# Optimization experiments

Measured on AMD Instinct MI355X. Metric: run time of the kernel, lower is better.

The kernel has to match this reference:

```python
import jax, jax.numpy as jnp
import numpy as np

N = 100000
E = 1600000
IN_C = 128
HID = 256
K_EIG = 64
OUT_C = 16


def setup_inputs() -> dict:
    key = jax.random.key(0)
    ks = jax.random.split(key, 8)
    x = jax.random.normal(ks[0], (N, IN_C), dtype=jnp.float32)
    edge_index = jax.random.randint(ks[1], (2, E), 0, N)
    MLP_W = jax.random.normal(ks[2], (K_EIG, N), dtype=jnp.float32) * 0.02
    MLP_b = jax.random.normal(ks[3], (K_EIG,), dtype=jnp.float32) * 0.02
    mlpx_W = jax.random.normal(ks[4], (HID, IN_C), dtype=jnp.float32) * 0.05
    mlpx_b = jax.random.normal(ks[5], (HID,), dtype=jnp.float32) * 0.02
    fin_W = jax.random.normal(ks[6], (OUT_C, HID + K_EIG), dtype=jnp.float32) * 0.05
    fin_b = jax.random.normal(ks[7], (OUT_C,), dtype=jnp.float32) * 0.02
    return {"x": x, "edge_index": edge_index, "MLP_W": MLP_W, "MLP_b": MLP_b,
            "mlpx_W": mlpx_W, "mlpx_b": mlpx_b, "fin_W": fin_W, "fin_b": fin_b}


def _spmm(row, col, feats, n):
    # adj is COO with coords (col[e], row[e]) and value 1 -> out[col] += feats[row]
    return jax.ops.segment_sum(feats[row], col, num_segments=n)


def _pump(xA, row, col, n):
    # MinCut-style pump: soft assignment, normalized-cut loss + orthogonality loss
    S = jax.nn.softmax(xA, axis=-1)                      # [N, K]
    AS = _spmm(row, col, S, n)                            # A @ S, [N, K]
    cut = jnp.sum(S * AS)                                 # tr(S^T A S)
    deg = jax.ops.segment_sum(jnp.ones(col.shape, S.dtype), col, num_segments=n)
    deg_term = jnp.sum(deg[:, None] * S * S)              # tr(S^T D S)
    pump_loss = -(cut / deg_term)
    SS = S.T @ S                                          # [K, K]
    k = S.shape[1]
    ortho_loss = jnp.linalg.norm(SS / jnp.linalg.norm(SS)
                                 - jnp.eye(k, dtype=S.dtype) / jnp.sqrt(jnp.asarray(k, S.dtype)))
    return S, pump_loss, ortho_loss


def reference(x, edge_index, MLP_W, MLP_b, mlpx_W, mlpx_b, fin_W, fin_b):
    row, col = edge_index[0], edge_index[1]
    n = x.shape[0]
    # xA = adj @ MLP.weight.T + bias   (irregular gather/scatter over edges)
    xA = _spmm(row, col, MLP_W.T, n) + MLP_b              # [N, K]
    xX = x @ mlpx_W.T + mlpx_b                            # [N, HID]
    xA, pump_loss, ortho_loss = _pump(xA, row, col, n)
    z = jnp.concatenate([xX, xA], axis=1)                 # [N, HID+K]
    # dropout omitted (eval mode)
    z = jax.nn.log_softmax(z @ fin_W.T + fin_b, axis=-1)  # [N, OUT]
    return (z, pump_loss + ortho_loss)
```

## Files before the change

### kernel.cpp

```cpp
#include <hip/hip_runtime.h>
#include <math.h>

#define N_NODES 100000
#define N_EDGES 1600000
#define IN_C    128
#define HID     256
#define KEIG    64
#define OUT_C   16

#define NPB      256
#define NBUCKET  ((N_NODES + NPB - 1) / NPB)
#define EDGE_TILE 4096
#define NTILE    ((N_EDGES + EDGE_TILE - 1) / EDGE_TILE)
#define CAP      8960

#define TRANS_BLOCKS   ((N_NODES + 63) / 64)
#define GATHER_BLOCKS  2048
#define CUT_BLOCKS     2048
#define SSP_BLOCKS     512
#define OUTG_BLOCKS    384
#define TAIL_BLOCKS    (128 * 23)

typedef __attribute__((ext_vector_type(8))) short short8;
typedef __attribute__((ext_vector_type(4))) float f32x4;
typedef __attribute__((ext_vector_type(2))) float f32x2;

__device__ __forceinline__ float wave_sum(float v) {
#pragma unroll
    for (int m = 32; m; m >>= 1) v += __shfl_xor(v, m, 64);
    return v;
}
__device__ __forceinline__ float bf2f(unsigned int u) {
    return __uint_as_float((u & 0xffffu) << 16);
}
__device__ __forceinline__ unsigned short f2bf(float f) {
    unsigned int u = __float_as_uint(f);
    u += 0x7fff + ((u >> 16) & 1);
    return (unsigned short)(u >> 16);
}
__device__ __forceinline__ unsigned char f2fp8(float f) {
    int p = __builtin_amdgcn_cvt_pk_fp8_f32(f, f, 0, false);
    return (unsigned char)(p & 0xff);
}

#define FMA4(P, s, W) \
    P.x = fmaf(s, W.x, P.x); P.y = fmaf(s, W.y, P.y); \
    P.z = fmaf(s, W.z, P.z); P.w = fmaf(s, W.w, P.w);

#define GSEL(RR) (q == 0 ? RR.x : q == 1 ? RR.y : q == 2 ? RR.z : RR.w)

#define GATHER4V(TBL, DST) do {                                                  \
    int4 ra_ = *(const int4*)(csr_row + ps + j);                                 \
    int r0_ = GSEL(ra_);                                                         \
    unsigned u0_ = *(const unsigned*)(TBL + (unsigned)r0_ * 64u + cb);           \
    f32x2 p_;                                                                    \
    p_ = __builtin_amdgcn_cvt_pk_f32_fp8(u0_, false); DST.x += p_.x; DST.y += p_.y; \
    p_ = __builtin_amdgcn_cvt_pk_f32_fp8(u0_, true);  DST.z += p_.x; DST.w += p_.y; \
} while (0)

#define GATHER16V(TBL, DST) do {                                                 \
    int4 ra_ = *(const int4*)(csr_row + ps + j);                                 \
    int4 rb_ = *(const int4*)(csr_row + ps + j + 4);                             \
    int4 rc_ = *(const int4*)(csr_row + ps + j + 8);                             \
    int4 rd_ = *(const int4*)(csr_row + ps + j + 12);                            \
    int r0_ = GSEL(ra_), r1_ = GSEL(rb_), r2_ = GSEL(rc_), r3_ = GSEL(rd_);      \
    unsigned u0_ = *(const unsigned*)(TBL + (unsigned)r0_ * 64u + cb);           \
    unsigned u1_ = *(const unsigned*)(TBL + (unsigned)r1_ * 64u + cb);           \
    unsigned u2_ = *(const unsigned*)(TBL + (unsigned)r2_ * 64u + cb);           \
    unsigned u3_ = *(const unsigned*)(TBL + (unsigned)r3_ * 64u + cb);           \
    f32x2 p_;                                                                    \
    p_ = __builtin_amdgcn_cvt_pk_f32_fp8(u0_, false); DST.x += p_.x; DST.y += p_.y; \
    p_ = __builtin_amdgcn_cvt_pk_f32_fp8(u0_, true);  DST.z += p_.x; DST.w += p_.y; \
    p_ = __builtin_amdgcn_cvt_pk_f32_fp8(u1_, false); DST.x += p_.x; DST.y += p_.y; \
    p_ = __builtin_amdgcn_cvt_pk_f32_fp8(u1_, true);  DST.z += p_.x; DST.w += p_.y; \
    p_ = __builtin_amdgcn_cvt_pk_f32_fp8(u2_, false); DST.x += p_.x; DST.y += p_.y; \
    p_ = __builtin_amdgcn_cvt_pk_f32_fp8(u2_, true);  DST.z += p_.x; DST.w += p_.y; \
    p_ = __builtin_amdgcn_cvt_pk_f32_fp8(u3_, false); DST.x += p_.x; DST.y += p_.y; \
    p_ = __builtin_amdgcn_cvt_pk_f32_fp8(u3_, true);  DST.z += p_.x; DST.w += p_.y; \
} while (0)

__global__ void prep_weff(const float* __restrict__ mlpxW, const float* __restrict__ mlpxb,
                          const float* __restrict__ finW, const float* __restrict__ finb,
                          float* __restrict__ Weff, float* __restrict__ beff,
                          int* __restrict__ bcnt, unsigned char* __restrict__ WT8,
                          unsigned char* __restrict__ S8, int* __restrict__ gpad) {
    int t = blockIdx.x * blockDim.x + threadIdx.x;
    const int NW = (IN_C + KEIG) * OUT_C;
    if (t < NW) {
        int k = t >> 4, o = t & 15;
        float acc;
        if (k < IN_C) {
            acc = 0.f;
            for (int c = 0; c < HID; ++c)
                acc += mlpxW[c * IN_C + k] * finW[o * (HID + KEIG) + c];
        } else {
            acc = finW[o * (HID + KEIG) + HID + (k - IN_C)];
        }
        Weff[k * OUT_C + o] = acc;
    }
    int tb = t - NW;
    if (tb >= 0 && tb < OUT_C) {
        float acc = finb[tb];
        for (int c = 0; c < HID; ++c) acc += mlpxb[c] * finW[tb * (HID + KEIG) + c];
        beff[tb] = acc;
    }
    int tz = t - (NW + OUT_C);
    if (tz >= 0 && tz <= NBUCKET) bcnt[tz] = 0;
    int tp = t - (NW + OUT_C + NBUCKET + 1);
    if (tp >= 0 && tp < 16) {
        ((int*)(WT8 + (size_t)N_NODES * 64))[tp] = 0;
        ((int*)(S8 + (size_t)N_NODES * 64))[tp] = 0;
        if (tp == 0) *gpad = 0;
    }
}

__global__ __launch_bounds__(256) void fused_prep(const float* __restrict__ W,
                                                  unsigned char* __restrict__ WT8,
                                                  const int* __restrict__ ei,
                                                  int* __restrict__ bcnt) {
    __shared__ __align__(16) char sm[64 * 65 * 4];
    int t = threadIdx.x;
    if (blockIdx.x < TRANS_BLOCKS) {
        float (*tile)[65] = (float (*)[65])sm;
        int n0 = blockIdx.x * 64;
        int tn = t & 63, tq = t >> 6;
#pragma unroll
        for (int kk = 0; kk < 16; ++kk) {
            int k = tq * 16 + kk;
            int n = n0 + tn;
            tile[k][tn] = (n < N_NODES) ? W[(long long)k * N_NODES + n] : 0.f;
        }
        __syncthreads();
        int tk = t & 63;
#pragma unroll
        for (int ii = 0; ii < 16; ++ii) {
            int n = n0 + tq * 16 + ii;
            if (n < N_NODES) WT8[(unsigned)n * 64u + tk] = f2fp8(tile[tk][tq * 16 + ii] * 32.f);
        }
    } else {
        int* h = (int*)sm;
        for (int i = t; i < NBUCKET; i += 256) h[i] = 0;
        __syncthreads();
        int tile_i = blockIdx.x - TRANS_BLOCKS;
        int e0 = tile_i * EDGE_TILE;
        int e1 = min(e0 + EDGE_TILE, N_EDGES);
        for (int e = e0 + t; e < e1; e += 256)
            atomicAdd(&h[ei[N_EDGES + e] >> 8], 1);
        __syncthreads();
        for (int i = t; i < NBUCKET; i += 256)
            if (h[i]) atomicAdd(&bcnt[i], h[i]);
    }
}

__global__ void bucket_scan(const int* __restrict__ bcnt, int* __restrict__ bbase,
                            int* __restrict__ bcur) {
    __shared__ int sh[512];
    int t = threadIdx.x;
    int v = (t < NBUCKET) ? bcnt[t] : 0;
    sh[t] = v;
    __syncthreads();
    for (int d = 1; d < 512; d <<= 1) {
        int u = (t >= d) ? sh[t - d] : 0;
        __syncthreads();
        sh[t] += u;
        __syncthreads();
    }
    if (t < NBUCKET) { bbase[t] = sh[t] - v; bcur[t] = sh[t] - v; }
    if (t == 0) bbase[NBUCKET] = N_EDGES;
}

__global__ void bucket_scatter(const int* __restrict__ ei, int* __restrict__ bcur,
                               int* __restrict__ ebuf) {
    __shared__ int h[NBUCKET];
    __shared__ int gb[NBUCKET];
    __shared__ int lpre[NBUCKET];
    __shared__ int psum[256];
    __shared__ int stage[EDGE_TILE];
    __shared__ short bkt[EDGE_TILE];
    int t = threadIdx.x;
    for (int i = t; i < NBUCKET; i += 256) h[i] = 0;
    __syncthreads();
    int e0 = blockIdx.x * EDGE_TILE;
    int e1 = min(e0 + EDGE_TILE, N_EDGES);
    int nt = e1 - e0;
    for (int e = e0 + t; e < e1; e += 256)
        atomicAdd(&h[ei[N_EDGES + e] >> 8], 1);
    __syncthreads();
    int a0 = (2 * t < NBUCKET) ? h[2 * t] : 0;
    int a1 = (2 * t + 1 < NBUCKET) ? h[2 * t + 1] : 0;
    psum[t] = a0 + a1;
    __syncthreads();
    for (int d = 1; d < 256; d <<= 1) {
        int u = (t >= d) ? psum[t - d] : 0;
        __syncthreads();
        psum[t] += u;
        __syncthreads();
    }
    int base = (t == 0) ? 0 : psum[t - 1];
    if (2 * t < NBUCKET) lpre[2 * t] = base;
    if (2 * t + 1 < NBUCKET) lpre[2 * t + 1] = base + a0;
    __syncthreads();
    for (int i = t; i < NBUCKET; i += 256) {
        int c = h[i];
        gb[i] = c ? atomicAdd(&bcur[i], c) : 0;
        h[i] = lpre[i];
    }
    __syncthreads();
    for (int e = e0 + t; e < e1; e += 256) {
        int r = ei[e];
        int c = ei[N_EDGES + e];
        int b = c >> 8;
        int slot = atomicAdd(&h[b], 1);
        stage[slot] = r | ((c & 255) << 17);
        bkt[slot] = (short)b;
    }
    __syncthreads();
    for (int s = t; s < nt; s += 256) {
        int b = bkt[s];
        ebuf[gb[b] + s - lpre[b]] = stage[s];
    }
}

__global__ void csr_build(const int* __restrict__ ebuf, const int* __restrict__ bbase,
                          int2* __restrict__ nodei,
                          int* __restrict__ csr_row, int* __restrict__ gpad) {
    __shared__ int hist[NPB];
    __shared__ int sh[NPB];
    __shared__ int curs[NPB];
    __shared__ int staged[CAP];
    __shared__ int pbase_sh;
    int b = blockIdx.x;
    int t = threadIdx.x;
    int s0 = bbase[b], s1 = bbase[b + 1];
    hist[t] = 0;
    __syncthreads();
    for (int i = s0 + t; i < s1; i += 256)
        atomicAdd(&hist[ebuf[i] >> 17], 1);
    __syncthreads();
    int v = hist[t];
    int pv = (v + 3) & ~3;
    sh[t] = pv;
    __syncthreads();
    for (int d = 1; d < 256; d <<= 1) {
        int u = (t >= d) ? sh[t - d] : 0;
        __syncthreads();
        sh[t] += u;
        __syncthreads();
    }
    int pexcl = sh[t] - pv;
    int pt = sh[255];
    if (t == 0) pbase_sh = atomicAdd(gpad, pt);
    __syncthreads();
    int pbase = pbase_sh;
    int node = b * NPB + t;
    if (node < N_NODES) nodei[node] = make_int2(v, pbase + pexcl);
    curs[t] = pexcl;
    __syncthreads();
    if (pt <= CAP) {
        for (int i = t; i < pt; i += 256) staged[i] = N_NODES;
        __syncthreads();
        for (int i = s0 + t; i < s1; i += 256) {
            int pk = ebuf[i];
            int pos = atomicAdd(&curs[pk >> 17], 1);
            staged[pos] = pk & 0x1FFFF;
        }
        __syncthreads();
        for (int i = t; i < pt; i += 256) csr_row[pbase + i] = staged[i];
    } else {
        for (int i = t; i < pt; i += 256) csr_row[pbase + i] = N_NODES;
        __syncthreads();
        for (int i = s0 + t; i < s1; i += 256) {
            int pk = ebuf[i];
            int pos = atomicAdd(&curs[pk >> 17], 1);
            csr_row[pbase + pos] = pk & 0x1FFFF;
        }
    }
}

__global__ void gather_softmax(const int2* __restrict__ nodei,
                               const int* __restrict__ csr_row,
                               const unsigned char* __restrict__ WT8,
                               const float* __restrict__ MLPb,
                               unsigned short* __restrict__ Sb,
                               unsigned char* __restrict__ S8,
                               float* __restrict__ dtp) {
    int lane = threadIdx.x & 63;
    int q = lane >> 4;
    unsigned cb = (unsigned)(lane & 15) * 4u;
    int wib = __builtin_amdgcn_readfirstlane(threadIdx.x >> 6);
    int gw = blockIdx.x * 4 + wib;
    int nw = gridDim.x * 4;
    f32x4 bias = *(const f32x4*)(MLPb + (lane & 15) * 4);
    float dacc = 0.f;
    for (int n = gw; n < N_NODES; n += nw) {
        int2 di = nodei[n];
        int deg = __builtin_amdgcn_readfirstlane(di.x);
        int ps  = __builtin_amdgcn_readfirstlane(di.y);
        int plen = (deg + 3) & ~3;
        f32x4 acc = {0.f, 0.f, 0.f, 0.f};
        int j = 0;
        for (; j + 16 <= plen; j += 16) { GATHER16V(WT8, acc); }
        for (; j < plen; j += 4) { GATHER4V(WT8, acc); }
#pragma unroll
        for (int mm = 16; mm < 64; mm <<= 1) {
            acc.x += __shfl_xor(acc.x, mm, 64);
            acc.y += __shfl_xor(acc.y, mm, 64);
            acc.z += __shfl_xor(acc.z, mm, 64);
            acc.w += __shfl_xor(acc.w, mm, 64);
        }
        float ax = bias.x + acc.x * 0.03125f;
        float ay = bias.y + acc.y * 0.03125f;
        float az = bias.z + acc.z * 0.03125f;
        float aw = bias.w + acc.w * 0.03125f;
        float m4 = fmaxf(fmaxf(ax, ay), fmaxf(az, aw));
#pragma unroll
        for (int mm = 1; mm < 16; mm <<= 1) m4 = fmaxf(m4, __shfl_xor(m4, mm, 64));
        float ex = __expf(ax - m4), ey = __expf(ay - m4);
        float ez = __expf(az - m4), ew = __expf(aw - m4);
        float s4 = (ex + ey) + (ez + ew);
#pragma unroll
        for (int mm = 1; mm < 16; mm <<= 1) s4 += __shfl_xor(s4, mm, 64);
        float inv = 1.f / s4;
        float sx = ex * inv, sy = ey * inv, sz = ez * inv, sw = ew * inv;
        if (q == 0) {
            unsigned lo = (unsigned)f2bf(sx) | ((unsigned)f2bf(sy) << 16);
            unsigned hi = (unsigned)f2bf(sz) | ((unsigned)f2bf(sw) << 16);
            *(uint2*)(Sb + (unsigned)n * 64u + cb) = make_uint2(lo, hi);
            int p8 = __builtin_amdgcn_cvt_pk_fp8_f32(sx * 64.f, sy * 64.f, 0, false);
            p8 = __builtin_amdgcn_cvt_pk_fp8_f32(sz * 64.f, sw * 64.f, p8, true);
            *(unsigned*)(S8 + (unsigned)n * 64u + cb) = (unsigned)p8;
        }
        dacc += (float)deg * ((sx * sx + sy * sy) + (sz * sz + sw * sw));
    }
    dacc = wave_sum(dacc);
    __shared__ float red[4];
    if (lane == 0) red[wib] = dacc * 0.25f;
    __syncthreads();
    if (threadIdx.x == 0) dtp[blockIdx.x] = red[0] + red[1] + red[2] + red[3];
}

__global__ __launch_bounds__(256) void fused_tail(
        const int2* __restrict__ nodei,
        const int* __restrict__ csr_row,
        const unsigned short* __restrict__ Sb, const unsigned char* __restrict__ S8,
        float* __restrict__ cutp, float* __restrict__ ssp,
        const float* __restrict__ x, const float* __restrict__ Weff,
        const float* __restrict__ beff, float* __restrict__ out) {
    __shared__ __align__(16) char sm[768 * 16 + 64];
    int t = threadIdx.x;
    int grp = blockIdx.x / 23;
    int r23 = blockIdx.x % 23;

    if (r23 < 16) {
        int bid = grp * 16 + r23;
        int lane = t & 63;
        int q = lane >> 4;
        unsigned cb = (unsigned)(lane & 15) * 4u;
        int wib = __builtin_amdgcn_readfirstlane(t >> 6);
        int gw = bid * 4 + wib;
        int nw = CUT_BLOCKS * 4;
        float acc = 0.f;
        for (int n = gw; n < N_NODES; n += nw) {
            int2 di = nodei[n];
            int deg = __builtin_amdgcn_readfirstlane(di.x);
            int ps  = __builtin_amdgcn_readfirstlane(di.y);
            uint2 su = *(const uint2*)(Sb + (unsigned)n * 64u + cb);
            int plen = (deg + 3) & ~3;
            f32x4 g = {0.f, 0.f, 0.f, 0.f};
            int j = 0;
            for (; j + 16 <= plen; j += 16) { GATHER16V(S8, g); }
            for (; j < plen; j += 4) { GATHER4V(S8, g); }
            acc += bf2f(su.x) * g.x + bf2f(su.x >> 16) * g.y
                 + bf2f(su.y) * g.z + bf2f(su.y >> 16) * g.w;
        }
        acc = wave_sum(acc);
        float* red = (float*)sm;
        if (lane == 0) red[wib] = acc * 0.015625f;
        __syncthreads();
        if (t == 0) cutp[bid] = red[0] + red[1] + red[2] + red[3];
    } else if (r23 < 20) {
        int bid2 = grp * 4 + (r23 - 16);
        unsigned short (*Sr)[66] = (unsigned short (*)[66])sm;
        int lane = t & 63;
        int w = t >> 6;
        int m = lane & 15;
        int quad = lane >> 4;
        int srow = t >> 3;
        int spart = t & 7;
        f32x4 a0 = {0.f,0.f,0.f,0.f}, a1 = {0.f,0.f,0.f,0.f};
        f32x4 a2 = {0.f,0.f,0.f,0.f}, a3 = {0.f,0.f,0.f,0.f};
        for (int base = bid2 * 32; base < N_NODES; base += SSP_BLOCKS * 32) {
            const uint4* g = (const uint4*)(Sb + (long long)(base + srow) * 64 + spart * 8);
            uint4 d = *g;
            __syncthreads();
            unsigned int* rowp = (unsigned int*)&Sr[srow][0];
            rowp[spart * 4 + 0] = d.x;
            rowp[spart * 4 + 1] = d.y;
            rowp[spart * 4 + 2] = d.z;
            rowp[spart * 4 + 3] = d.w;
            __syncthreads();
            short8 f0, f1, f2, f3;
#pragma unroll
            for (int j = 0; j < 8; ++j) {
                int k = quad * 8 + j;
                f0[j] = (short)Sr[k][m];
                f1[j] = (short)Sr[k][16 + m];
                f2[j] = (short)Sr[k][32 + m];
                f3[j] = (short)Sr[k][48 + m];
            }
            short8 fa = (w == 0) ? f0 : (w == 1) ? f1 : (w == 2) ? f2 : f3;
            a0 = __builtin_amdgcn_mfma_f32_16x16x32_bf16(fa, f0, a0, 0, 0, 0);
            a1 = __builtin_amdgcn_mfma_f32_16x16x32_bf16(fa, f1, a1, 0, 0, 0);
            a2 = __builtin_amdgcn_mfma_f32_16x16x32_bf16(fa, f2, a2, 0, 0, 0);
            a3 = __builtin_amdgcn_mfma_f32_16x16x32_bf16(fa, f3, a3, 0, 0, 0);
        }
        float* dst = ssp + (size_t)bid2 * 4096;
#pragma unroll
        for (int r = 0; r < 4; ++r) {
            int row = w * 16 + quad * 4 + r;
            dst[row * 64 +  0 + m] = a0[r];
            dst[row * 64 + 16 + m] = a1[r];
            dst[row * 64 + 32 + m] = a2[r];
            dst[row * 64 + 48 + m] = a3[r];
        }
    } else {
        int obid = grp * 3 + (r23 - 20);
        float4* Wsh = (float4*)sm;
        float* bsh = (float*)(sm + 768 * 16);
        const float4* W4 = (const float4*)Weff;
        for (int i = t; i < 768; i += 256) Wsh[i] = W4[i];
        if (t < 16) bsh[t] = beff[t];
        __syncthreads();
        for (int r = obid * 256 + t; r < N_NODES; r += OUTG_BLOCKS * 256) {
            float4 p0 = make_float4(bsh[0], bsh[1], bsh[2], bsh[3]);
            float4 p1 = make_float4(bsh[4], bsh[5], bsh[6], bsh[7]);
            float4 p2 = make_float4(bsh[8], bsh[9], bsh[10], bsh[11]);
            float4 p3 = make_float4(bsh[12], bsh[13], bsh[14], bsh[15]);
            const float4* xr = (const float4*)(x + (long long)r * IN_C);
#pragma unroll 8
            for (int j = 0; j < 32; ++j) {
                float4 xv = xr[j];
                int k = j * 4;
                float xs[4] = {xv.x, xv.y, xv.z, xv.w};
#pragma unroll
                for (int c = 0; c < 4; ++c) {
                    float s = xs[c];
                    float4 w0 = Wsh[(k + c) * 4 + 0];
                    float4 w1 = Wsh[(k + c) * 4 + 1];
                    float4 w2 = Wsh[(k + c) * 4 + 2];
                    float4 w3 = Wsh[(k + c) * 4 + 3];
                    FMA4(p0, s, w0); FMA4(p1, s, w1); FMA4(p2, s, w2); FMA4(p3, s, w3);
                }
            }
            const uint2* sr = (const uint2*)(Sb + (long long)r * 64);
#pragma unroll 8
            for (int j = 0; j < 16; ++j) {
                uint2 u = sr[j];
                float xs[4] = {bf2f(u.x), bf2f(u.x >> 16), bf2f(u.y), bf2f(u.y >> 16)};
                int k = IN_C + j * 4;
#pragma unroll
                for (int c = 0; c < 4; ++c) {
                    float s = xs[c];
                    float4 w0 = Wsh[(k + c) * 4 + 0];
                    float4 w1 = Wsh[(k + c) * 4 + 1];
                    float4 w2 = Wsh[(k + c) * 4 + 2];
                    float4 w3 = Wsh[(k + c) * 4 + 3];
                    FMA4(p0, s, w0); FMA4(p1, s, w1); FMA4(p2, s, w2); FMA4(p3, s, w3);
                }
            }
            float m = fmaxf(fmaxf(fmaxf(p0.x, p0.y), fmaxf(p0.z, p0.w)),
                            fmaxf(fmaxf(fmaxf(p1.x, p1.y), fmaxf(p1.z, p1.w)),
                                  fmaxf(fmaxf(fmaxf(p2.x, p2.y), fmaxf(p2.z, p2.w)),
                                        fmaxf(fmaxf(p3.x, p3.y), fmaxf(p3.z, p3.w)))));
            float sum = __expf(p0.x - m) + __expf(p0.y - m) + __expf(p0.z - m) + __expf(p0.w - m)
                      + __expf(p1.x - m) + __expf(p1.y - m) + __expf(p1.z - m) + __expf(p1.w - m)
                      + __expf(p2.x - m) + __expf(p2.y - m) + __expf(p2.z - m) + __expf(p2.w - m)
                      + __expf(p3.x - m) + __expf(p3.y - m) + __expf(p3.z - m) + __expf(p3.w - m);
            float lse = m + logf(sum);
            float4* o4 = (float4*)(out + (long long)r * OUT_C);
            o4[0] = make_float4(p0.x - lse, p0.y - lse, p0.z - lse, p0.w - lse);
            o4[1] = make_float4(p1.x - lse, p1.y - lse, p1.z - lse, p1.w - lse);
            o4[2] = make_float4(p2.x - lse, p2.y - lse, p2.z - lse, p2.w - lse);
            o4[3] = make_float4(p3.x - lse, p3.y - lse, p3.z - lse, p3.w - lse);
        }
    }
}

__global__ void reduce_ss(const float* __restrict__ ssp, float* __restrict__ SS) {
    int e = blockIdx.x * blockDim.x + threadIdx.x;
    float s = 0.f;
    for (int p = 0; p < SSP_BLOCKS; ++p) s += ssp[(size_t)p * 4096 + e];
    SS[e] = s;
}

__global__ void scalars_kernel(const float* __restrict__ cutp, const float* __restrict__ dtp,
                               const float* __restrict__ SS, float* __restrict__ out) {
    __shared__ float red[256];
    int t = threadIdx.x;
    float c = 0.f;
    for (int i = t; i < CUT_BLOCKS; i += 256) c += cutp[i];
    red[t] = c; __syncthreads();
    for (int s = 128; s; s >>= 1) { if (t < s) red[t] += red[t + s]; __syncthreads(); }
    float cut = red[0]; __syncthreads();

    float d = 0.f;
    for (int i = t; i < GATHER_BLOCKS; i += 256) d += dtp[i];
    red[t] = d; __syncthreads();
    for (int s = 128; s; s >>= 1) { if (t < s) red[t] += red[t + s]; __syncthreads(); }
    float dterm = red[0]; __syncthreads();

    float ss[16];
    float sq = 0.f;
#pragma unroll
    for (int j = 0; j < 16; ++j) { ss[j] = SS[t * 16 + j]; sq += ss[j] * ss[j]; }
    red[t] = sq; __syncthreads();
    for (int s = 128; s; s >>= 1) { if (t < s) red[t] += red[t + s]; __syncthreads(); }
    float nrm = sqrtf(red[0]); __syncthreads();

    float osq = 0.f;
#pragma unroll
    for (int j = 0; j < 16; ++j) {
        int idx = t * 16 + j;
        float v = ss[j] / nrm - ((idx % 65 == 0) ? 0.125f : 0.f);
        osq += v * v;
    }
    red[t] = osq; __syncthreads();
    for (int s = 128; s; s >>= 1) { if (t < s) red[t] += red[t + s]; __syncthreads(); }
    if (t == 0) {
        float loss = -(cut / dterm) + sqrtf(red[0]);
        out[(long long)N_NODES * OUT_C] = loss;
    }
}

extern "C" void kernel_launch(void* const* d_in, const int* in_sizes, int n_in,
                              void* d_out, int out_size, void* d_ws, size_t ws_size,
                              hipStream_t stream) {
    const float* x     = (const float*)d_in[0];
    const int*   ei    = (const int*)d_in[1];
    const float* MLPW  = (const float*)d_in[2];
    const float* MLPb  = (const float*)d_in[3];
    const float* mlpxW = (const float*)d_in[4];
    const float* mlpxb = (const float*)d_in[5];
    const float* finW  = (const float*)d_in[6];
    const float* finb  = (const float*)d_in[7];
    float* out = (float*)d_out;
    char* ws = (char*)d_ws;

    unsigned char*  WT8 = (unsigned char*)ws;
    unsigned char*  S8  = (unsigned char*)(ws + (size_t)(N_NODES + 1) * 64);
    unsigned short* Sb  = (unsigned short*)(ws + (size_t)(N_NODES + 1) * 128);
    char* p = ws + (size_t)(N_NODES + 1) * 128 + (size_t)N_NODES * 128;
    float* ssp  = (float*)p;
    float* SS   = ssp + (size_t)SSP_BLOCKS * 4096;
    float* Weff = SS + 4096;
    float* beff = Weff + 192 * 16;
    float* cutp = beff + 16;
    float* dtp  = cutp + CUT_BLOCKS;
    int* ebuf    = (int*)(dtp + GATHER_BLOCKS);
    int* csr_row = ebuf + N_EDGES;
    int2* nodei  = (int2*)(csr_row + N_EDGES + 16 * N_NODES);
    int* bcnt    = (int*)(nodei + N_NODES);
    int* bbase   = bcnt + NBUCKET + 1;
    int* bcur    = bbase + NBUCKET + 1;
    int* gpad    = bcur + NBUCKET;

    hipLaunchKernelGGL(prep_weff, dim3(16), dim3(256), 0, stream,
                       mlpxW, mlpxb, finW, finb, Weff, beff, bcnt, WT8, S8, gpad);
    hipLaunchKernelGGL(fused_prep, dim3(TRANS_BLOCKS + NTILE), dim3(256), 0, stream,
                       MLPW, WT8, ei, bcnt);
    hipLaunchKernelGGL(bucket_scan, dim3(1), dim3(512), 0, stream, bcnt, bbase, bcur);
    hipLaunchKernelGGL(bucket_scatter, dim3(NTILE), dim3(256), 0, stream, ei, bcur, ebuf);
    hipLaunchKernelGGL(csr_build, dim3(NBUCKET), dim3(256), 0, stream,
                       ebuf, bbase, nodei, csr_row, gpad);
    hipLaunchKernelGGL(gather_softmax, dim3(GATHER_BLOCKS), dim3(256), 0, stream,
                       nodei, csr_row, WT8, MLPb, Sb, S8, dtp);
    hipLaunchKernelGGL(fused_tail, dim3(TAIL_BLOCKS), dim3(256), 0, stream,
                       nodei, csr_row, Sb, S8, cutp, ssp, x, Weff, beff, out);
    hipLaunchKernelGGL(reduce_ss, dim3(16), dim3(256), 0, stream, ssp, SS);
    hipLaunchKernelGGL(scalars_kernel, dim3(1), dim3(256), 0, stream, cutp, dtp, SS, out);
}
```

Before: 305.2 us.

## Software-pipeline CSR gathers over contiguous 16-node wave chunks with 16-padded rows

The gather kernels stop striding one node per wave. Each wave now owns a contiguous chunk of 16 nodes whose padded CSR rows form one run, and it walks that run in groups of 16 edges. Index loads are prefetched two groups ahead and table loads one group ahead, which hides the latency of the dependent index-then-row loads. CSR row padding goes from 4 to 16, the grid sizes and tail block split are rebalanced, and launch bounds are added. The larger padding adds wasted sentinel gathers for low-degree nodes, and contiguous chunking can cause load imbalance across waves.

```diff
diff --git a/kernel.cpp b/kernel.cpp
--- a/kernel.cpp
+++ b/kernel.cpp
@@ -15,11 +15,12 @@
 #define CAP      8960
 
 #define TRANS_BLOCKS   ((N_NODES + 63) / 64)
-#define GATHER_BLOCKS  2048
-#define CUT_BLOCKS     2048
-#define SSP_BLOCKS     512
-#define OUTG_BLOCKS    384
-#define TAIL_BLOCKS    (128 * 23)
+#define GATHER_BLOCKS  ((N_NODES + 63) / 64)
+#define CUT_VB         1573
+#define SSP_BLOCKS     484
+#define SSP_ALLOC      512
+#define OUTG_BLOCKS    363
+#define TAIL_BLOCKS    (121 * 20)
 
 typedef __attribute__((ext_vector_type(8))) short short8;
 typedef __attribute__((ext_vector_type(4))) float f32x4;
@@ -47,36 +48,15 @@
     P.x = fmaf(s, W.x, P.x); P.y = fmaf(s, W.y, P.y); \
     P.z = fmaf(s, W.z, P.z); P.w = fmaf(s, W.w, P.w);
 
-#define GSEL(RR) (q == 0 ? RR.x : q == 1 ? RR.y : q == 2 ? RR.z : RR.w)
-
-#define GATHER4V(TBL, DST) do {                                                  \
-    int4 ra_ = *(const int4*)(csr_row + ps + j);                                 \
-    int r0_ = GSEL(ra_);                                                         \
-    unsigned u0_ = *(const unsigned*)(TBL + (unsigned)r0_ * 64u + cb);           \
-    f32x2 p_;                                                                    \
-    p_ = __builtin_amdgcn_cvt_pk_f32_fp8(u0_, false); DST.x += p_.x; DST.y += p_.y; \
-    p_ = __builtin_amdgcn_cvt_pk_f32_fp8(u0_, true);  DST.z += p_.x; DST.w += p_.y; \
-} while (0)
-
-#define GATHER16V(TBL, DST) do {                                                 \
-    int4 ra_ = *(const int4*)(csr_row + ps + j);                                 \
-    int4 rb_ = *(const int4*)(csr_row + ps + j + 4);                             \
-    int4 rc_ = *(const int4*)(csr_row + ps + j + 8);                             \
-    int4 rd_ = *(const int4*)(csr_row + ps + j + 12);                            \
-    int r0_ = GSEL(ra_), r1_ = GSEL(rb_), r2_ = GSEL(rc_), r3_ = GSEL(rd_);      \
-    unsigned u0_ = *(const unsigned*)(TBL + (unsigned)r0_ * 64u + cb);           \
-    unsigned u1_ = *(const unsigned*)(TBL + (unsigned)r1_ * 64u + cb);           \
-    unsigned u2_ = *(const unsigned*)(TBL + (unsigned)r2_ * 64u + cb);           \
-    unsigned u3_ = *(const unsigned*)(TBL + (unsigned)r3_ * 64u + cb);           \
-    f32x2 p_;                                                                    \
-    p_ = __builtin_amdgcn_cvt_pk_f32_fp8(u0_, false); DST.x += p_.x; DST.y += p_.y; \
-    p_ = __builtin_amdgcn_cvt_pk_f32_fp8(u0_, true);  DST.z += p_.x; DST.w += p_.y; \
-    p_ = __builtin_amdgcn_cvt_pk_f32_fp8(u1_, false); DST.x += p_.x; DST.y += p_.y; \
-    p_ = __builtin_amdgcn_cvt_pk_f32_fp8(u1_, true);  DST.z += p_.x; DST.w += p_.y; \
-    p_ = __builtin_amdgcn_cvt_pk_f32_fp8(u2_, false); DST.x += p_.x; DST.y += p_.y; \
-    p_ = __builtin_amdgcn_cvt_pk_f32_fp8(u2_, true);  DST.z += p_.x; DST.w += p_.y; \
-    p_ = __builtin_amdgcn_cvt_pk_f32_fp8(u3_, false); DST.x += p_.x; DST.y += p_.y; \
-    p_ = __builtin_amdgcn_cvt_pk_f32_fp8(u3_, true);  DST.z += p_.x; DST.w += p_.y; \
+#define CONS4(ACC) do { f32x2 p_;                                                   \
+    p_ = __builtin_amdgcn_cvt_pk_f32_fp8(uA0, false); ACC.x += p_.x; ACC.y += p_.y; \
+    p_ = __builtin_amdgcn_cvt_pk_f32_fp8(uA0, true);  ACC.z += p_.x; ACC.w += p_.y; \
+    p_ = __builtin_amdgcn_cvt_pk_f32_fp8(uA1, false); ACC.x += p_.x; ACC.y += p_.y; \
+    p_ = __builtin_amdgcn_cvt_pk_f32_fp8(uA1, true);  ACC.z += p_.x; ACC.w += p_.y; \
+    p_ = __builtin_amdgcn_cvt_pk_f32_fp8(uA2, false); ACC.x += p_.x; ACC.y += p_.y; \
+    p_ = __builtin_amdgcn_cvt_pk_f32_fp8(uA2, true);  ACC.z += p_.x; ACC.w += p_.y; \
+    p_ = __builtin_amdgcn_cvt_pk_f32_fp8(uA3, false); ACC.x += p_.x; ACC.y += p_.y; \
+    p_ = __builtin_amdgcn_cvt_pk_f32_fp8(uA3, true);  ACC.z += p_.x; ACC.w += p_.y; \
 } while (0)
 
 __global__ void prep_weff(const float* __restrict__ mlpxW, const float* __restrict__ mlpxb,
@@ -238,7 +218,7 @@
         atomicAdd(&hist[ebuf[i] >> 17], 1);
     __syncthreads();
     int v = hist[t];
-    int pv = (v + 3) & ~3;
+    int pv = (v + 15) & ~15;
     sh[t] = pv;
     __syncthreads();
     for (int d = 1; d < 256; d <<= 1) {
@@ -277,60 +257,86 @@
     }
 }
 
-__global__ void gather_softmax(const int2* __restrict__ nodei,
-                               const int* __restrict__ csr_row,
-                               const unsigned char* __restrict__ WT8,
-                               const float* __restrict__ MLPb,
-                               unsigned short* __restrict__ Sb,
-                               unsigned char* __restrict__ S8,
-                               float* __restrict__ dtp) {
+__global__ __launch_bounds__(256, 4) void gather_softmax(
+        const int2* __restrict__ nodei, const int* __restrict__ csr_row,
+        const unsigned char* __restrict__ WT8, const float* __restrict__ MLPb,
+        unsigned short* __restrict__ Sb, unsigned char* __restrict__ S8,
+        float* __restrict__ dtp) {
     int lane = threadIdx.x & 63;
     int q = lane >> 4;
-    unsigned cb = (unsigned)(lane & 15) * 4u;
+    int c = lane & 15;
+    unsigned cb = (unsigned)c * 4u;
     int wib = __builtin_amdgcn_readfirstlane(threadIdx.x >> 6);
-    int gw = blockIdx.x * 4 + wib;
-    int nw = gridDim.x * 4;
-    f32x4 bias = *(const f32x4*)(MLPb + (lane & 15) * 4);
+    int n0 = (blockIdx.x * 4 + wib) * 16;
     float dacc = 0.f;
-    for (int n = gw; n < N_NODES; n += nw) {
-        int2 di = nodei[n];
-        int deg = __builtin_amdgcn_readfirstlane(di.x);
-        int ps  = __builtin_amdgcn_readfirstlane(di.y);
-        int plen = (deg + 3) & ~3;
-        f32x4 acc = {0.f, 0.f, 0.f, 0.f};
-        int j = 0;
-        for (; j + 16 <= plen; j += 16) { GATHER16V(WT8, acc); }
-        for (; j < plen; j += 4) { GATHER4V(WT8, acc); }
-#pragma unroll
-        for (int mm = 16; mm < 64; mm <<= 1) {
-            acc.x += __shfl_xor(acc.x, mm, 64);
-            acc.y += __shfl_xor(acc.y, mm, 64);
-            acc.z += __shfl_xor(acc.z, mm, 64);
-            acc.w += __shfl_xor(acc.w, mm, 64);
-        }
-        float ax = bias.x + acc.x * 0.03125f;
-        float ay = bias.y + acc.y * 0.03125f;
-        float az = bias.z + acc.z * 0.03125f;
-        float aw = bias.w + acc.w * 0.03125f;
-        float m4 = fmaxf(fmaxf(ax, ay), fmaxf(az, aw));
-#pragma unroll
-        for (int mm = 1; mm < 16; mm <<= 1) m4 = fmaxf(m4, __shfl_xor(m4, mm, 64));
-        float ex = __expf(ax - m4), ey = __expf(ay - m4);
-        float ez = __expf(az - m4), ew = __expf(aw - m4);
-        float s4 = (ex + ey) + (ez + ew);
-#pragma unroll
-        for (int mm = 1; mm < 16; mm <<= 1) s4 += __shfl_xor(s4, mm, 64);
-        float inv = 1.f / s4;
-        float sx = ex * inv, sy = ey * inv, sz = ez * inv, sw = ew * inv;
-        if (q == 0) {
-            unsigned lo = (unsigned)f2bf(sx) | ((unsigned)f2bf(sy) << 16);
-            unsigned hi = (unsigned)f2bf(sz) | ((unsigned)f2bf(sw) << 16);
-            *(uint2*)(Sb + (unsigned)n * 64u + cb) = make_uint2(lo, hi);
-            int p8 = __builtin_amdgcn_cvt_pk_fp8_f32(sx * 64.f, sy * 64.f, 0, false);
-            p8 = __builtin_amdgcn_cvt_pk_fp8_f32(sz * 64.f, sw * 64.f, p8, true);
-            *(unsigned*)(S8 + (unsigned)n * 64u + cb) = (unsigned)p8;
-        }
-        dacc += (float)deg * ((sx * sx + sy * sy) + (sz * sz + sw * sw));
+    if (n0 < N_NODES) {
+        int nvalid = min(16, N_NODES - n0);
+        int2 di = nodei[n0 + min(c, nvalid - 1)];
+        f32x4 bias = *(const f32x4*)(MLPb + c * 4);
+        int ps0  = __shfl(di.y, 0, 64);
+        int degL = __shfl(di.x, nvalid - 1, 64);
+        int psL  = __shfl(di.y, nvalid - 1, 64);
+        int G = ((psL + ((degL + 15) & ~15)) - ps0) >> 4;
+        const int* cw = csr_row + ps0 + (q << 2);
+        int4 iB = {0, 0, 0, 0};
+        unsigned uA0 = 0, uA1 = 0, uA2 = 0, uA3 = 0;
+        if (G > 0) {
+            int4 iA = *(const int4*)(cw);
+            uA0 = *(const unsigned*)(WT8 + (unsigned)iA.x * 64u + cb);
+            uA1 = *(const unsigned*)(WT8 + (unsigned)iA.y * 64u + cb);
+            uA2 = *(const unsigned*)(WT8 + (unsigned)iA.z * 64u + cb);
+            uA3 = *(const unsigned*)(WT8 + (unsigned)iA.w * 64u + cb);
+            int g1 = (G > 1) ? 1 : 0;
+            iB = *(const int4*)(cw + (g1 << 4));
+        }
+        int g = 0;
+        for (int k = 0; k < nvalid; ++k) {
+            int deg = __shfl(di.x, k, 64);
+            int gcnt = (deg + 15) >> 4;
+            f32x4 acc = {0.f, 0.f, 0.f, 0.f};
+            for (int tt = 0; tt < gcnt; ++tt) {
+                int gn = g + 2; if (gn >= G) gn = G - 1;
+                int4 iC = *(const int4*)(cw + (gn << 4));
+                unsigned uB0 = *(const unsigned*)(WT8 + (unsigned)iB.x * 64u + cb);
+                unsigned uB1 = *(const unsigned*)(WT8 + (unsigned)iB.y * 64u + cb);
+                unsigned uB2 = *(const unsigned*)(WT8 + (unsigned)iB.z * 64u + cb);
+                unsigned uB3 = *(const unsigned*)(WT8 + (unsigned)iB.w * 64u + cb);
+                CONS4(acc);
+                uA0 = uB0; uA1 = uB1; uA2 = uB2; uA3 = uB3; iB = iC;
+                ++g;
+            }
+#pragma unroll
+            for (int mm = 16; mm < 64; mm <<= 1) {
+                acc.x += __shfl_xor(acc.x, mm, 64);
+                acc.y += __shfl_xor(acc.y, mm, 64);
+                acc.z += __shfl_xor(acc.z, mm, 64);
+                acc.w += __shfl_xor(acc.w, mm, 64);
+            }
+            float ax = bias.x + acc.x * 0.03125f;
+            float ay = bias.y + acc.y * 0.03125f;
+            float az = bias.z + acc.z * 0.03125f;
+            float aw = bias.w + acc.w * 0.03125f;
+            float m4 = fmaxf(fmaxf(ax, ay), fmaxf(az, aw));
+#pragma unroll
+            for (int mm = 1; mm < 16; mm <<= 1) m4 = fmaxf(m4, __shfl_xor(m4, mm, 64));
+            float ex = __expf(ax - m4), ey = __expf(ay - m4);
+            float ez = __expf(az - m4), ew = __expf(aw - m4);
+            float s4 = (ex + ey) + (ez + ew);
+#pragma unroll
+            for (int mm = 1; mm < 16; mm <<= 1) s4 += __shfl_xor(s4, mm, 64);
+            float inv = 1.f / s4;
+            float sx = ex * inv, sy = ey * inv, sz = ez * inv, sw = ew * inv;
+            if (q == 0) {
+                unsigned nidx = (unsigned)(n0 + k);
+                unsigned lo = (unsigned)f2bf(sx) | ((unsigned)f2bf(sy) << 16);
+                unsigned hi = (unsigned)f2bf(sz) | ((unsigned)f2bf(sw) << 16);
+                *(uint2*)(Sb + nidx * 64u + cb) = make_uint2(lo, hi);
+                int p8 = __builtin_amdgcn_cvt_pk_fp8_f32(sx * 64.f, sy * 64.f, 0, false);
+                p8 = __builtin_amdgcn_cvt_pk_fp8_f32(sz * 64.f, sw * 64.f, p8, true);
+                *(unsigned*)(S8 + nidx * 64u + cb) = (unsigned)p8;
+            }
+            dacc += (float)deg * ((sx * sx + sy * sy) + (sz * sz + sw * sw));
+        }
     }
     dacc = wave_sum(dacc);
     __shared__ float red[4];
@@ -339,7 +345,7 @@
     if (threadIdx.x == 0) dtp[blockIdx.x] = red[0] + red[1] + red[2] + red[3];
 }
 
-__global__ __launch_bounds__(256) void fused_tail(
+__global__ __launch_bounds__(256, 4) void fused_tail(
         const int2* __restrict__ nodei,
         const int* __restrict__ csr_row,
         const unsigned short* __restrict__ Sb, const unsigned char* __restrict__ S8,
@@ -348,38 +354,67 @@
         const float* __restrict__ beff, float* __restrict__ out) {
     __shared__ __align__(16) char sm[768 * 16 + 64];
     int t = threadIdx.x;
-    int grp = blockIdx.x / 23;
-    int r23 = blockIdx.x % 23;
-
-    if (r23 < 16) {
-        int bid = grp * 16 + r23;
+    int grp = blockIdx.x / 20;
+    int r20 = blockIdx.x % 20;
+
+    if (r20 < 13) {
+        int vb = grp * 13 + r20;
         int lane = t & 63;
         int q = lane >> 4;
-        unsigned cb = (unsigned)(lane & 15) * 4u;
+        int c = lane & 15;
+        unsigned cb = (unsigned)c * 4u;
         int wib = __builtin_amdgcn_readfirstlane(t >> 6);
-        int gw = bid * 4 + wib;
-        int nw = CUT_BLOCKS * 4;
-        float acc = 0.f;
-        for (int n = gw; n < N_NODES; n += nw) {
-            int2 di = nodei[n];
-            int deg = __builtin_amdgcn_readfirstlane(di.x);
-            int ps  = __builtin_amdgcn_readfirstlane(di.y);
-            uint2 su = *(const uint2*)(Sb + (unsigned)n * 64u + cb);
-            int plen = (deg + 3) & ~3;
-            f32x4 g = {0.f, 0.f, 0.f, 0.f};
-            int j = 0;
-            for (; j + 16 <= plen; j += 16) { GATHER16V(S8, g); }
-            for (; j < plen; j += 4) { GATHER4V(S8, g); }
-            acc += bf2f(su.x) * g.x + bf2f(su.x >> 16) * g.y
-                 + bf2f(su.y) * g.z + bf2f(su.y >> 16) * g.w;
-        }
-        acc = wave_sum(acc);
+        int n0 = vb * 64 + wib * 16;
+        float cacc = 0.f;
+        if (n0 < N_NODES) {
+            int nvalid = min(16, N_NODES - n0);
+            int2 di = nodei[n0 + min(c, nvalid - 1)];
+            int ps0  = __shfl(di.y, 0, 64);
+            int degL = __shfl(di.x, nvalid - 1, 64);
+            int psL  = __shfl(di.y, nvalid - 1, 64);
+            int G = ((psL + ((degL + 15) & ~15)) - ps0) >> 4;
+            const int* cw = csr_row + ps0 + (q << 2);
+            uint2 suA = *(const uint2*)(Sb + (unsigned)n0 * 64u + cb);
+            int4 iB = {0, 0, 0, 0};
+            unsigned uA0 = 0, uA1 = 0, uA2 = 0, uA3 = 0;
+            if (G > 0) {
+                int4 iA = *(const int4*)(cw);
+                uA0 = *(const unsigned*)(S8 + (unsigned)iA.x * 64u + cb);
+                uA1 = *(const unsigned*)(S8 + (unsigned)iA.y * 64u + cb);
+                uA2 = *(const unsigned*)(S8 + (unsigned)iA.z * 64u + cb);
+                uA3 = *(const unsigned*)(S8 + (unsigned)iA.w * 64u + cb);
+                int g1 = (G > 1) ? 1 : 0;
+                iB = *(const int4*)(cw + (g1 << 4));
+            }
+            int g = 0;
+            for (int k = 0; k < nvalid; ++k) {
+                int deg = __shfl(di.x, k, 64);
+                int gcnt = (deg + 15) >> 4;
+                uint2 suN = *(const uint2*)(Sb + (unsigned)(n0 + min(k + 1, nvalid - 1)) * 64u + cb);
+                f32x4 acc = {0.f, 0.f, 0.f, 0.f};
+                for (int tt = 0; tt < gcnt; ++tt) {
+                    int gn = g + 2; if (gn >= G) gn = G - 1;
+                    int4 iC = *(const int4*)(cw + (gn << 4));
+                    unsigned uB0 = *(const unsigned*)(S8 + (unsigned)iB.x * 64u + cb);
+                    unsigned uB1 = *(const unsigned*)(S8 + (unsigned)iB.y * 64u + cb);
+                    unsigned uB2 = *(const unsigned*)(S8 + (unsigned)iB.z * 64u + cb);
+                    unsigned uB3 = *(const unsigned*)(S8 + (unsigned)iB.w * 64u + cb);
+                    CONS4(acc);
+                    uA0 = uB0; uA1 = uB1; uA2 = uB2; uA3 = uB3; iB = iC;
+                    ++g;
+                }
+                cacc += bf2f(suA.x) * acc.x + bf2f(suA.x >> 16) * acc.y
+                      + bf2f(suA.y) * acc.z + bf2f(suA.y >> 16) * acc.w;
+                suA = suN;
+            }
+        }
+        cacc = wave_sum(cacc);
         float* red = (float*)sm;
-        if (lane == 0) red[wib] = acc * 0.015625f;
-        __syncthreads();
-        if (t == 0) cutp[bid] = red[0] + red[1] + red[2] + red[3];
-    } else if (r23 < 20) {
-        int bid2 = grp * 4 + (r23 - 16);
+        if (lane == 0) red[wib] = cacc * 0.015625f;
+        __syncthreads();
+        if (t == 0) cutp[vb] = red[0] + red[1] + red[2] + red[3];
+    } else if (r20 < 17) {
+        int bid2 = grp * 4 + (r20 - 13);
         unsigned short (*Sr)[66] = (unsigned short (*)[66])sm;
         int lane = t & 63;
         int w = t >> 6;
@@ -424,7 +459,7 @@
             dst[row * 64 + 48 + m] = a3[r];
         }
     } else {
-        int obid = grp * 3 + (r23 - 20);
+        int obid = grp * 3 + (r20 - 17);
         float4* Wsh = (float4*)sm;
         float* bsh = (float*)(sm + 768 * 16);
         const float4* W4 = (const float4*)Weff;
@@ -498,7 +533,7 @@
     __shared__ float red[256];
     int t = threadIdx.x;
     float c = 0.f;
-    for (int i = t; i < CUT_BLOCKS; i += 256) c += cutp[i];
+    for (int i = t; i < CUT_VB; i += 256) c += cutp[i];
     red[t] = c; __syncthreads();
     for (int s = 128; s; s >>= 1) { if (t < s) red[t] += red[t + s]; __syncthreads(); }
     float cut = red[0]; __syncthreads();
@@ -551,12 +586,12 @@
     unsigned short* Sb  = (unsigned short*)(ws + (size_t)(N_NODES + 1) * 128);
     char* p = ws + (size_t)(N_NODES + 1) * 128 + (size_t)N_NODES * 128;
     float* ssp  = (float*)p;
-    float* SS   = ssp + (size_t)SSP_BLOCKS * 4096;
+    float* SS   = ssp + (size_t)SSP_ALLOC * 4096;
     float* Weff = SS + 4096;
     float* beff = Weff + 192 * 16;
     float* cutp = beff + 16;
-    float* dtp  = cutp + CUT_BLOCKS;
-    int* ebuf    = (int*)(dtp + GATHER_BLOCKS);
+    float* dtp  = cutp + 2048;
+    int* ebuf    = (int*)(dtp + 2048);
     int* csr_row = ebuf + N_EDGES;
     int2* nodei  = (int2*)(csr_row + N_EDGES + 16 * N_NODES);
     int* bcnt    = (int*)(nodei + N_NODES);
```

New measurement: 300.2 us. About the same (-1.7%).
